# Kernel tuning notes

Hardware: AMD Instinct MI355X
Metric: run time of the kernel (lower is better)

## Reference

```python
import jax
jax.config.update("jax_enable_x64", True)
import jax.numpy as jnp
import numpy as np

B, T, C, H = 4, 4096, 120, 64  # batch, seq, n_embed, head_size


def setup_inputs() -> dict:
    key = jax.random.key(0)
    kx, kk, kq, kv = jax.random.split(key, 4)
    x = jax.random.normal(kx, (B, T, C), dtype=jnp.float32)
    s = 1.0 / np.sqrt(C)  # ~nn.Linear init scale
    Wk = jax.random.normal(kk, (C, H), dtype=jnp.float32) * s
    Wq = jax.random.normal(kq, (C, H), dtype=jnp.float32) * s
    Wv = jax.random.normal(kv, (C, H), dtype=jnp.float32) * s
    return {"x": x, "Wk": Wk, "Wq": Wq, "Wv": Wv}


def reference(x, Wk, Wq, Wv):
    # Original module runs entirely in float64 (.double()).
    x = x.astype(jnp.float64)
    Wk = Wk.astype(jnp.float64)
    Wq = Wq.astype(jnp.float64)
    Wv = Wv.astype(jnp.float64)
    k = jnp.einsum("btc,ch->bth", x, Wk)
    q = jnp.einsum("btc,ch->bth", x, Wq)
    v = jnp.einsum("btc,ch->bth", x, Wv)
    scale = x.shape[-1] ** (-0.5)  # NOTE: scales by n_embed (C), not head_size
    wei = jnp.einsum("bth,bsh->bts", q, k) * scale  # [B, T, T]
    wei = jax.nn.softmax(wei, axis=-1)
    # dropout(p=0.01) is identity in eval mode
    out = jnp.einsum("bts,bsh->bth", wei, v)  # [B, T, H]
    return out
```

## Files before the change

kernel.cpp:

```cpp
#include <hip/hip_runtime.h>

typedef __attribute__((ext_vector_type(2))) float f32x2;
typedef __attribute__((ext_vector_type(4))) float f32x4;
typedef __attribute__((ext_vector_type(8))) short s16x8;
typedef __attribute__((ext_vector_type(2))) unsigned int u32x2;
typedef __attribute__((ext_vector_type(4))) unsigned int u32x4;

#define BN 4
#define TN 4096
#define CN 120
#define HN 64

__device__ __forceinline__ unsigned short f2bf(float f) {
  unsigned int u = __float_as_uint(f);
  unsigned int r = (u + 0x7fffu + ((u >> 16) & 1u)) >> 16;
  return (unsigned short)r;
}
__device__ __forceinline__ float bf2f(unsigned short h) {
  return __uint_as_float((unsigned int)h << 16);
}
__device__ __forceinline__ float fast_exp2(float x) {
#if __has_builtin(__builtin_amdgcn_exp2f)
  return __builtin_amdgcn_exp2f(x);
#else
  return exp2f(x);
#endif
}


__global__ __launch_bounds__(256, 3) void proj_kernel(
    const float* __restrict__ x, const float* __restrict__ Wk,
    const float* __restrict__ Wq, const float* __restrict__ Wv,
    unsigned short* __restrict__ Kf, unsigned short* __restrict__ Qg,
    unsigned short* __restrict__ Vf) {
  __shared__ struct {
    unsigned short xh[64][136];
    unsigned short xl[64][136];
    unsigned short vt[64][72];
  } sm;
  const int tid = threadIdx.x;
  const int mat = blockIdx.x >> 8;
  const int rb = blockIdx.x & 255;
  const int row0 = rb * 64;
  const int wave = tid >> 6, lane = tid & 63;
  const int l15 = lane & 15, quad = lane >> 4;
  const int b = row0 >> 12, key0 = row0 & (TN - 1);

  const float* Ws = (mat == 0) ? Wk : (mat == 1) ? Wq : Wv;
  const float wsc = (mat == 1) ? 0.13169944f : 1.0f;
  s16x8 wh[4], wl[4];
#pragma unroll
  for (int kc = 0; kc < 4; ++kc) {
#pragma unroll
    for (int j = 0; j < 8; ++j) {
      const int c = kc * 32 + quad * 8 + j;
      const float w = (c < CN) ? Ws[c * HN + wave * 16 + l15] * wsc : 0.f;
      const unsigned short h16 = f2bf(w);
      wh[kc][j] = (short)h16;
      wl[kc][j] = (short)f2bf(w - bf2f(h16));
    }
  }

  for (int n = tid; n < 64 * 30; n += 256) {
    const int row = n / 30, c4 = n - row * 30;
    const f32x4 xv = *(const f32x4*)&x[(size_t)(row0 + row) * CN + c4 * 4];
    u32x2 hp, lp;
#pragma unroll
    for (int e = 0; e < 2; ++e) {
      const unsigned short h0 = f2bf(xv[2 * e]);
      const unsigned short h1 = f2bf(xv[2 * e + 1]);
      hp[e] = (unsigned int)h0 | ((unsigned int)h1 << 16);
      lp[e] = (unsigned int)f2bf(xv[2 * e] - bf2f(h0)) |
              ((unsigned int)f2bf(xv[2 * e + 1] - bf2f(h1)) << 16);
    }
    *(u32x2*)&sm.xh[row][c4 * 4] = hp;
    *(u32x2*)&sm.xl[row][c4 * 4] = lp;
  }
  if (tid < 64) {
    const u32x4 z = {0u, 0u, 0u, 0u};
    *(u32x4*)&sm.xh[tid][120] = z;
    *(u32x4*)&sm.xl[tid][120] = z;
  }
  __syncthreads();

  f32x4 acc[4];
#pragma unroll
  for (int mt = 0; mt < 4; ++mt) acc[mt] = 0.f;
#pragma unroll
  for (int mt = 0; mt < 4; ++mt) {
#pragma unroll
    for (int kc = 0; kc < 4; ++kc) {
      const s16x8 ah = *(const s16x8*)&sm.xh[mt * 16 + l15][kc * 32 + quad * 8];
      const s16x8 al = *(const s16x8*)&sm.xl[mt * 16 + l15][kc * 32 + quad * 8];
      acc[mt] = __builtin_amdgcn_mfma_f32_16x16x32_bf16(al, wh[kc], acc[mt], 0, 0, 0);
      acc[mt] = __builtin_amdgcn_mfma_f32_16x16x32_bf16(ah, wl[kc], acc[mt], 0, 0, 0);
      acc[mt] = __builtin_amdgcn_mfma_f32_16x16x32_bf16(ah, wh[kc], acc[mt], 0, 0, 0);
    }
  }

  if (mat < 2) {
#pragma unroll
    for (int mt = 0; mt < 4; ++mt)
#pragma unroll
      for (int r = 0; r < 4; ++r)
        sm.vt[mt * 16 + quad * 4 + r][wave * 16 + l15] = f2bf(acc[mt][r]);
    __syncthreads();
    if (mat == 1) {
      const int row = tid >> 2, seg = tid & 3;
      const u32x4 d0 = *(const u32x4*)&sm.vt[row][seg * 16];
      const u32x4 d1 = *(const u32x4*)&sm.vt[row][seg * 16 + 8];
      unsigned short* qp = &Qg[(size_t)(row0 + row) * HN + seg * 16];
      *(u32x4*)qp = d0;
      *(u32x4*)(qp + 8) = d1;
    } else {
#pragma unroll
      for (int i = 0; i < 2; ++i) {
        const int c = tid + i * 256;
        const int ktl = c >> 7, ch = (c >> 6) & 1, L = c & 63;
        const u32x4 d =
            *(const u32x4*)&sm.vt[ktl * 16 + (L & 15)][(L >> 4) * 8 + ch * 32];
        *(u32x4*)((unsigned char*)Kf +
                  (((size_t)b * 256 + (key0 >> 4) + ktl) * 128 + ch * 64 + L) *
                      16) = d;
      }
    }
  } else {
#pragma unroll
    for (int mt = 0; mt < 4; ++mt)
#pragma unroll
      for (int r = 0; r < 4; ++r)
        sm.vt[wave * 16 + l15][mt * 16 + quad * 4 + r] = f2bf(acc[mt][r]);
    __syncthreads();
#pragma unroll
    for (int i = 0; i < 2; ++i) {
      const int c = tid + i * 256;
      const int kbl = c >> 8, ht = (c >> 6) & 3, L = c & 63;
      const u32x4 d =
          *(const u32x4*)&sm.vt[ht * 16 + (L & 15)][kbl * 32 + (L >> 4) * 8];
      *(u32x4*)((unsigned char*)Vf +
                (((size_t)b * 128 + (key0 >> 5) + kbl) * 4 + ht) * 1024 +
                L * 16) = d;
    }
  }
}

__global__ __launch_bounds__(512, 4) void attn_kernel(
    const unsigned short* __restrict__ Qg, const unsigned short* __restrict__ Kf,
    const unsigned short* __restrict__ Vf, float* __restrict__ out) {
  __shared__ union {
    unsigned short p[8][2][16][72];
    struct { float ob[8][64][17]; float lb[8][16]; } m;
  } sm;
  const int bid = blockIdx.x;
  const int xslot = bid & 7;
  const int b = xslot >> 1;
  const int qt5 = (bid >> 3) | ((xslot & 1) << 6);
  const int qbase = qt5 * 32;
  const int tid = threadIdx.x;
  const int wave = tid >> 6, lane = tid & 63;
  const int l15 = lane & 15, quad = lane >> 4;

  s16x8 qf[2][2];
#pragma unroll
  for (int qt = 0; qt < 2; ++qt) {
    const unsigned short* qrow =
        Qg + (size_t)(b * TN + qbase + qt * 16 + l15) * HN + quad * 8;
    qf[qt][0] = *(const s16x8*)qrow;
    qf[qt][1] = *(const s16x8*)(qrow + 32);
  }

  const unsigned char* Kfb = (const unsigned char*)Kf + (size_t)b * 524288;
  const unsigned char* Vfb = (const unsigned char*)Vf + (size_t)b * 524288;
  char* pw[2];
#pragma unroll
  for (int qt = 0; qt < 2; ++qt)
    pw[qt] = (char*)&sm.p[wave][qt][0][0] + l15 * 144;

  f32x4 o[2][4];
#pragma unroll
  for (int qt = 0; qt < 2; ++qt)
#pragma unroll
    for (int t = 0; t < 4; ++t) o[qt][t] = 0.f;
  f32x2 la2[2];
  la2[0] = 0.f;
  la2[1] = 0.f;

  const int kb0 = wave * 512;
#pragma unroll 1
  for (int it = 0; it < 8; ++it) {
    const int kb = kb0 + it * 64;
#pragma unroll
    for (int t = 0; t < 4; ++t) {
      const unsigned char* ktp =
          Kfb + (size_t)((kb >> 4) + t) * 2048 + lane * 16;
      const s16x8 a0 = *(const s16x8*)ktp;
      const s16x8 a1 = *(const s16x8*)(ktp + 1024);
      f32x4 s0 = 0.f, s1 = 0.f;
      __builtin_amdgcn_s_setprio(1);
      s0 = __builtin_amdgcn_mfma_f32_16x16x32_bf16(a0, qf[0][0], s0, 0, 0, 0);
      s0 = __builtin_amdgcn_mfma_f32_16x16x32_bf16(a1, qf[0][1], s0, 0, 0, 0);
      s1 = __builtin_amdgcn_mfma_f32_16x16x32_bf16(a0, qf[1][0], s1, 0, 0, 0);
      s1 = __builtin_amdgcn_mfma_f32_16x16x32_bf16(a1, qf[1][1], s1, 0, 0, 0);
      __builtin_amdgcn_s_setprio(0);
#pragma unroll
      for (int qt = 0; qt < 2; ++qt) {
        const f32x4 s = qt ? s1 : s0;
        const unsigned int u0 = __float_as_uint(fast_exp2(s[0]));
        const unsigned int u1 = __float_as_uint(fast_exp2(s[1]));
        const unsigned int u2 = __float_as_uint(fast_exp2(s[2]));
        const unsigned int u3 = __float_as_uint(fast_exp2(s[3]));
        const unsigned int m0 = u0 & 0xffff0000u, m1 = u1 & 0xffff0000u;
        const unsigned int m2 = u2 & 0xffff0000u, m3 = u3 & 0xffff0000u;
        f32x2 pa, pb;
        pa.x = __uint_as_float(m0);
        pa.y = __uint_as_float(m1);
        pb.x = __uint_as_float(m2);
        pb.y = __uint_as_float(m3);
        la2[qt] += pa + pb;
        u32x2 w;
        w.x = __builtin_amdgcn_perm(u1, u0, 0x07060302u);
        w.y = __builtin_amdgcn_perm(u3, u2, 0x07060302u);
        *(u32x2*)(pw[qt] + t * 32 + quad * 8) = w;
      }
    }
#pragma unroll 1
    for (int kc = 0; kc < 2; ++kc) {
      const s16x8 pb0 = *(const s16x8*)(pw[0] + quad * 16 + kc * 64);
      const s16x8 pb1 = *(const s16x8*)(pw[1] + quad * 16 + kc * 64);
#pragma unroll
      for (int ht = 0; ht < 4; ++ht) {
        const unsigned char* vtp =
            Vfb + (size_t)((kb >> 5) + kc) * 4096 + ht * 1024 + lane * 16;
        const s16x8 va = *(const s16x8*)vtp;
        __builtin_amdgcn_s_setprio(1);
        o[0][ht] = __builtin_amdgcn_mfma_f32_16x16x32_bf16(va, pb0, o[0][ht], 0, 0, 0);
        o[1][ht] = __builtin_amdgcn_mfma_f32_16x16x32_bf16(va, pb1, o[1][ht], 0, 0, 0);
        __builtin_amdgcn_s_setprio(0);
      }
    }
  }
  float lacc[2];
#pragma unroll
  for (int qt = 0; qt < 2; ++qt) {
    lacc[qt] = la2[qt].x + la2[qt].y;
    lacc[qt] += __shfl_xor(lacc[qt], 16, 64);
    lacc[qt] += __shfl_xor(lacc[qt], 32, 64);
  }
  __syncthreads();
#pragma unroll
  for (int qt = 0; qt < 2; ++qt) {
    if (lane < 16) sm.m.lb[wave][l15] = lacc[qt];
#pragma unroll
    for (int ht = 0; ht < 4; ++ht)
#pragma unroll
      for (int r = 0; r < 4; ++r)
        sm.m.ob[wave][ht * 16 + quad * 4 + r][l15] = o[qt][ht][r];
    __syncthreads();
    const int h = tid & 63;
    const int wq = tid >> 6;
#pragma unroll
    for (int i = 0; i < 2; ++i) {
      const int qq = (i << 3) | wq;
      float ssum = 0.f, ll = 0.f;
#pragma unroll
      for (int w = 0; w < 8; ++w) {
        ssum += sm.m.ob[w][h][qq];
        ll += sm.m.lb[w][qq];
      }
      out[(size_t)(b * TN + qbase + qt * 16 + qq) * HN + h] = ssum / ll;
    }
    __syncthreads();
  }
}

extern "C" void kernel_launch(void* const* d_in, const int* in_sizes, int n_in,
                              void* d_out, int out_size, void* d_ws,
                              size_t ws_size, hipStream_t stream) {
  const float* x = (const float*)d_in[0];
  const float* Wk = (const float*)d_in[1];
  const float* Wq = (const float*)d_in[2];
  const float* Wv = (const float*)d_in[3];
  unsigned short* Kf = (unsigned short*)d_ws;
  unsigned short* Qg = Kf + (size_t)BN * TN * HN;
  unsigned short* Vf = Qg + (size_t)BN * TN * HN;
  float* out = (float*)d_out;
  proj_kernel<<<768, 256, 0, stream>>>(x, Wk, Wq, Wv, Kf, Qg, Vf);
  attn_kernel<<<BN * TN / 32, 512, 0, stream>>>(Qg, Kf, Vf, out);
}
```

Before: 104.1 us.

## Split attention keys across 16 waves per block with dynamic LDS

Doubles the attention block to 1024 threads (16 waves), so each wave covers 256 keys instead of 512. The final cross-wave reduction now sums over 16 partial outputs, with one query row per wave. The static shared union is replaced by 72 KB of dynamic LDS, enabled through hipFuncSetAttribute. The s_setprio hints around the MFMAs are removed. The aim is more latency hiding per query tile, at the cost of a larger reduction and a tighter register budget implied by launch_bounds(1024,8).

```diff
diff --git a/kernel.cpp b/kernel.cpp
--- a/kernel.cpp
+++ b/kernel.cpp
@@ -144,13 +144,10 @@
   }
 }
 
-__global__ __launch_bounds__(512, 4) void attn_kernel(
+__global__ __launch_bounds__(1024, 8) void attn_kernel(
     const unsigned short* __restrict__ Qg, const unsigned short* __restrict__ Kf,
     const unsigned short* __restrict__ Vf, float* __restrict__ out) {
-  __shared__ union {
-    unsigned short p[8][2][16][72];
-    struct { float ob[8][64][17]; float lb[8][16]; } m;
-  } sm;
+  extern __shared__ unsigned char smraw[];
   const int bid = blockIdx.x;
   const int xslot = bid & 7;
   const int b = xslot >> 1;
@@ -174,7 +171,7 @@
   char* pw[2];
 #pragma unroll
   for (int qt = 0; qt < 2; ++qt)
-    pw[qt] = (char*)&sm.p[wave][qt][0][0] + l15 * 144;
+    pw[qt] = (char*)smraw + (wave * 2 + qt) * 2304 + l15 * 144;
 
   f32x4 o[2][4];
 #pragma unroll
@@ -185,9 +182,9 @@
   la2[0] = 0.f;
   la2[1] = 0.f;
 
-  const int kb0 = wave * 512;
+  const int kb0 = wave * 256;
 #pragma unroll 1
-  for (int it = 0; it < 8; ++it) {
+  for (int it = 0; it < 4; ++it) {
     const int kb = kb0 + it * 64;
 #pragma unroll
     for (int t = 0; t < 4; ++t) {
@@ -196,12 +193,10 @@
       const s16x8 a0 = *(const s16x8*)ktp;
       const s16x8 a1 = *(const s16x8*)(ktp + 1024);
       f32x4 s0 = 0.f, s1 = 0.f;
-      __builtin_amdgcn_s_setprio(1);
       s0 = __builtin_amdgcn_mfma_f32_16x16x32_bf16(a0, qf[0][0], s0, 0, 0, 0);
       s0 = __builtin_amdgcn_mfma_f32_16x16x32_bf16(a1, qf[0][1], s0, 0, 0, 0);
       s1 = __builtin_amdgcn_mfma_f32_16x16x32_bf16(a0, qf[1][0], s1, 0, 0, 0);
       s1 = __builtin_amdgcn_mfma_f32_16x16x32_bf16(a1, qf[1][1], s1, 0, 0, 0);
-      __builtin_amdgcn_s_setprio(0);
 #pragma unroll
       for (int qt = 0; qt < 2; ++qt) {
         const f32x4 s = qt ? s1 : s0;
@@ -232,10 +227,8 @@
         const unsigned char* vtp =
             Vfb + (size_t)((kb >> 5) + kc) * 4096 + ht * 1024 + lane * 16;
         const s16x8 va = *(const s16x8*)vtp;
-        __builtin_amdgcn_s_setprio(1);
         o[0][ht] = __builtin_amdgcn_mfma_f32_16x16x32_bf16(va, pb0, o[0][ht], 0, 0, 0);
         o[1][ht] = __builtin_amdgcn_mfma_f32_16x16x32_bf16(va, pb1, o[1][ht], 0, 0, 0);
-        __builtin_amdgcn_s_setprio(0);
       }
     }
   }
@@ -247,28 +240,26 @@
     lacc[qt] += __shfl_xor(lacc[qt], 32, 64);
   }
   __syncthreads();
+  float* ob = (float*)smraw;
+  float* lb = (float*)(smraw + 16 * 64 * 17 * 4);
 #pragma unroll
   for (int qt = 0; qt < 2; ++qt) {
-    if (lane < 16) sm.m.lb[wave][l15] = lacc[qt];
+    if (lane < 16) lb[wave * 16 + l15] = lacc[qt];
 #pragma unroll
     for (int ht = 0; ht < 4; ++ht)
 #pragma unroll
       for (int r = 0; r < 4; ++r)
-        sm.m.ob[wave][ht * 16 + quad * 4 + r][l15] = o[qt][ht][r];
+        ob[(wave * 64 + ht * 16 + quad * 4 + r) * 17 + l15] = o[qt][ht][r];
     __syncthreads();
     const int h = tid & 63;
     const int wq = tid >> 6;
-#pragma unroll
-    for (int i = 0; i < 2; ++i) {
-      const int qq = (i << 3) | wq;
-      float ssum = 0.f, ll = 0.f;
-#pragma unroll
-      for (int w = 0; w < 8; ++w) {
-        ssum += sm.m.ob[w][h][qq];
-        ll += sm.m.lb[w][qq];
-      }
-      out[(size_t)(b * TN + qbase + qt * 16 + qq) * HN + h] = ssum / ll;
-    }
+    float ssum = 0.f, ll = 0.f;
+#pragma unroll
+    for (int w = 0; w < 16; ++w) {
+      ssum += ob[(w * 64 + h) * 17 + wq];
+      ll += lb[w * 16 + wq];
+    }
+    out[(size_t)(b * TN + qbase + qt * 16 + wq) * HN + h] = ssum / ll;
     __syncthreads();
   }
 }
@@ -284,6 +275,13 @@
   unsigned short* Qg = Kf + (size_t)BN * TN * HN;
   unsigned short* Vf = Qg + (size_t)BN * TN * HN;
   float* out = (float*)d_out;
+  static bool smset = false;
+  if (!smset) {
+    (void)hipFuncSetAttribute((const void*)attn_kernel,
+                              hipFuncAttributeMaxDynamicSharedMemorySize,
+                              73728);
+    smset = true;
+  }
   proj_kernel<<<768, 256, 0, stream>>>(x, Wk, Wq, Wv, Kf, Qg, Vf);
-  attn_kernel<<<BN * TN / 32, 512, 0, stream>>>(Qg, Kf, Vf, out);
-}
+  attn_kernel<<<BN * TN / 32, 1024, 73728, stream>>>(Qg, Kf, Vf, out);
+}
```

After: 317.1 us. 3.05x slower.
